# Kernel tuning notes

Measured on AMD Instinct MI355X. Metric: run time of the kernel, lower is better.

Reference implementation:

```python
import jax, jax.numpy as jnp
import numpy as np


def to_tb(r, size, base=4):
    # (B, size, size, size) -> (B, (size//base)^3, base, base, base)
    n = size // base
    r = r.reshape(-1, size, size, n, base)
    r = r.transpose(0, 1, 3, 2, 4)
    r = r.reshape(-1, size, n * n, base, base)
    r = r.transpose(0, 2, 1, 3, 4)
    return r.reshape(-1, n ** 3, base, base, base)


def from_tb(r, size, base=4):
    # inverse-ish of to_tb, ends with an extra (0,1,3,2) transpose as in source
    n = size // base
    r = r.reshape(-1, n * n, size, base, base)
    r = r.transpose(0, 2, 1, 3, 4)
    r = r.reshape(-1, size, size, n, base)
    r = r.transpose(0, 1, 3, 2, 4)
    r = r.reshape(-1, size, size, size)
    return r.transpose(0, 1, 3, 2)


def downscale(r, size):
    r = to_tb(r, size)  # base=4
    r = r.sum(axis=(2, 3, 4)) / 64.0
    r = r.reshape(-1, size // 4, size // 4, size // 4)
    return r.transpose(0, 3, 2, 1)


def setup_inputs() -> dict:
    key = jax.random.key(0)
    # (batch=2, level=4, 4, 4, 4^(3*4-2)) with 4*4*1048576 = 256^3 per slice
    x = jax.random.normal(key, (2, 4, 4, 4, 1048576), dtype=jnp.float32)
    return {"x": x}


def reference(x):
    level = x.shape[1]
    xt = jnp.transpose(x, (1, 0, 2, 3, 4))  # (level, batch, 4, 4, ...)
    batch = xt.shape[1]
    d2 = xt.shape[2]
    size_full = 4 ** level
    n3 = (4 ** (level - 1)) ** 3
    ret = []
    for i in range(level):
        r = xt[i]
        r = from_tb(r, size_full, 4 ** i)  # -> (batch, size, size, size)
        for k in range(i):
            r = downscale(r, 4 ** (level - k))
        for _ in range(i):
            r = jnp.tile(r, (1, 4, 4, 4))
        r = to_tb(r, size_full)  # (batch, n3, 4, 4, 4)
        ret.append(r.reshape(-1, n3, 64))
    out = jnp.stack(ret)  # (level, batch, n3, 64)
    out = out.transpose(1, 0, 2, 3).reshape(batch, -1, d2 ** 3)
    return out
```

## Files before the change

kernel.cpp:

```cpp
#include <hip/hip_runtime.h>


typedef float f4 __attribute__((ext_vector_type(4)));

__global__ __launch_bounds__(256) void k_reduce(const float* __restrict__ in,
                                                float* __restrict__ d1,
                                                float* __restrict__ p2,
                                                float* __restrict__ p3) {
    const int b = blockIdx.y;
    const int bx = blockIdx.x;
    const int tid = threadIdx.x;
    __shared__ float red[64];
    const f4* in4 = (const f4*)in;

    if (bx < 2048) {
        const int tlow = bx >> 1;
        const int kh = bx & 1;
        const long base4 = (long)b * 16777216 + 4194304;
        float acc[2] = {0.f, 0.f};
        for (int dz = 0; dz < 4; ++dz) {
            long rb = base4 + (long)(dz * 1024 + tlow) * 1024;
#pragma unroll
            for (int kk = 0; kk < 2; ++kk) {
                f4 v = __builtin_nontemporal_load(&in4[rb + (kh * 2 + kk) * 256 + tid]);
                acc[kk] += v.x + v.y + v.z + v.w;
            }
        }
#pragma unroll
        for (int kk = 0; kk < 2; ++kk) {
            acc[kk] += __shfl_xor(acc[kk], 4);
            acc[kk] += __shfl_xor(acc[kk], 8);
        }
        if ((tid & 12) == 0) {
            int yp = tlow >> 4;
            int zp = ((tlow & 15) << 2) + (tid & 3);
#pragma unroll
            for (int kk = 0; kk < 2; ++kk) {
                int xp = (kh * 2 + kk) * 16 + (tid >> 4);
                d1[b * 262144 + xp * 4096 + yp * 64 + zp] = acc[kk] * (1.0f / 64.0f);
            }
        }
    } else if (bx < 4096) {
        const int blk = bx - 2048;
        const int g = blk & 7, cell = blk >> 3;
        const int yp = cell >> 4, xp = cell & 15;
        const long base4 = (long)b * 16777216 + 2 * 4194304 + yp * 16384 + xp * 1024;
        float acc = 0.f;
        for (int dzi = 0; dzi < 2; ++dzi) {
            long rb = base4 + (long)(g * 2 + dzi) * 262144;
#pragma unroll
            for (int k = 0; k < 4; ++k) {
                f4 v = __builtin_nontemporal_load(&in4[rb + k * 256 + tid]);
                acc += v.x + v.y + v.z + v.w;
            }
        }
        acc += __shfl_xor(acc, 1);
        acc += __shfl_xor(acc, 2);
        if ((tid & 3) == 0) red[tid >> 2] = acc;
        __syncthreads();
        if (tid < 16) {
            float s = red[tid] + red[16 + tid] + red[32 + tid] + red[48 + tid];
            p2[(b * 8 + g) * 4096 + xp * 256 + yp * 16 + tid] = s;
        }
    } else {
        const int blk = bx - 4096;
        const int kc = blk & 7;
        const int orig = blk >> 3;
        const int xp = orig >> 6, hi = (orig >> 2) & 15, dxg = orig & 3;
        const long base4 = (long)b * 16777216 + 3 * 4194304 +
                           (long)hi * 262144 + xp * 65536 + dxg * 16384;
        float acc = 0.f;
        for (int kk = 0; kk < 8; ++kk) {
            f4 v = __builtin_nontemporal_load(&in4[base4 + (kc * 8 + kk) * 256 + tid]);
            acc += v.x + v.y + v.z + v.w;
        }
        acc += __shfl_xor(acc, 1);
        acc += __shfl_xor(acc, 2);
        acc += __shfl_xor(acc, 4);
        acc += __shfl_xor(acc, 8);
        if ((tid & 15) == 0) red[tid >> 4] = acc;
        __syncthreads();
        if (tid < 16) {
            int G = (hi * 4 + dxg) * 8 + kc;
            p3[((b * 4 + xp) * 512 + G) * 16 + tid] = red[tid];
        }
    }
}

__global__ __launch_bounds__(256) void k_combine(const float* __restrict__ p2,
                                                 const float* __restrict__ p3,
                                                 float* __restrict__ d2,
                                                 float* __restrict__ d3) {
    const int bid = blockIdx.x;
    const int tid = threadIdx.x;
    if (bid < 32) {
        int idx = bid * 256 + tid;
        int b = idx >> 12, r = idx & 4095;
        float s = 0.f;
#pragma unroll
        for (int g = 0; g < 8; ++g) s += p2[(b * 8 + g) * 4096 + r];
        d2[idx] = s * (1.0f / 4096.0f);
    } else {
        int v = bid - 32;
        int b = v >> 2, xp = v & 3;
        int c = tid & 15, gp = tid >> 4;
        const float* pb = p3 + (long)((b * 4 + xp) * 512) * 16 + c;
        float s = 0.f;
#pragma unroll
        for (int j = 0; j < 32; ++j) s += pb[(gp * 32 + j) * 16];
        __shared__ float red[256];
        red[gp * 16 + c] = s;
        __syncthreads();
        if (tid < 16) {
            float t = 0.f;
#pragma unroll
            for (int g = 0; g < 16; ++g) t += red[g * 16 + tid];
            d3[b * 64 + xp * 16 + tid] = t * (1.0f / 262144.0f);
        }
    }
}

__global__ __launch_bounds__(256) void k_perm(const float* __restrict__ in,
                                              float* __restrict__ out) {
    const int b = blockIdx.y;
    const int Y_hi = blockIdx.x >> 6, Z_hi = blockIdx.x & 63;
    const int tid = threadIdx.x;
    __shared__ float lds[16 * 260];
    const f4* in4 = (const f4*)in;
    f4* out4 = (f4*)out;
    const long in_b4 = (long)b * 16777216;
#pragma unroll
    for (int k = 0; k < 4; ++k) {
        int idx = k * 256 + tid;
        int r = idx >> 6;
        int col4 = idx & 63;
        int Y = Y_hi * 4 + (r >> 2), Z = Z_hi * 4 + (r & 3);
        f4 v = __builtin_nontemporal_load(&in4[in_b4 + (long)Y * 16384 + Z * 64 + col4]);
        *(f4*)&lds[r * 260 + col4 * 4] = v;
    }
    __syncthreads();
    const long out_b4 = (long)b * 16777216 + (long)Z_hi * 65536 + Y_hi * 1024;
#pragma unroll
    for (int k = 0; k < 4; ++k) {
        int idx = k * 256 + tid;
        int X = ((idx >> 4) << 2) + ((tid >> 2) & 3);
        int row0 = (tid & 3) * 4;
        f4 v;
        v.x = lds[(row0 + 0) * 260 + X];
        v.y = lds[(row0 + 1) * 260 + X];
        v.z = lds[(row0 + 2) * 260 + X];
        v.w = lds[(row0 + 3) * 260 + X];
        __builtin_nontemporal_store(v, &out4[out_b4 + idx]);
    }
}

__global__ __launch_bounds__(256) void k_bcast(const float* __restrict__ d1,
                                               const float* __restrict__ d2,
                                               const float* __restrict__ d3,
                                               float* __restrict__ out) {
    const int b = blockIdx.y;
    const int bx = blockIdx.x;
    const int tid = threadIdx.x;
    f4* out4 = (f4*)out;

    if (bx < 4096) {
        const f4* d14 = (const f4*)d1;
        const long ob = (long)b * 16777216 + 4194304;
        const int d1b = b * 65536;
#pragma unroll
        for (int k = 0; k < 4; ++k) {
            int o4 = bx * 1024 + k * 256 + tid;
            int u = o4 >> 4;
            int Xl = (o4 >> 2) & 3, Yl = o4 & 3;
            int Xh = u & 63, Yh = (u >> 6) & 63, Zh = u >> 12;
            int x = (Xh & 15) * 4 + Xl, y = (Yh & 15) * 4 + Yl;
            f4 v = d14[d1b + x * 1024 + y * 16 + (Zh & 15)];
            __builtin_nontemporal_store(v, &out4[ob + o4]);
        }
    } else if (bx < 8192) {
        const int blk = bx - 4096;
        const f4* d24 = (const f4*)d2;
        const long ob = (long)b * 16777216 + 2 * 4194304;
#pragma unroll
        for (int k = 0; k < 4; ++k) {
            int o4 = blk * 1024 + k * 256 + tid;
            int u = o4 >> 4;
            int Xl = (o4 >> 2) & 3, Yl = o4 & 3;
            int Xh = u & 63, Yh = (u >> 6) & 63, Zh = u >> 12;
            int x = (Xh & 3) * 4 + Xl, y = (Yh & 3) * 4 + Yl;
            f4 v = d24[b * 1024 + x * 64 + y * 4 + (Zh & 3)];
            __builtin_nontemporal_store(v, &out4[ob + o4]);
        }
    } else {
        const int blk = bx - 8192;
        const f4* d34 = (const f4*)d3;
        const f4 v = d34[b * 16 + (tid & 15)];
        const long ob = (long)b * 16777216 + 3 * 4194304;
#pragma unroll
        for (int k = 0; k < 4; ++k)
            __builtin_nontemporal_store(v, &out4[ob + blk * 1024 + k * 256 + tid]);
    }
}

extern "C" void kernel_launch(void* const* d_in, const int* in_sizes, int n_in,
                              void* d_out, int out_size, void* d_ws, size_t ws_size,
                              hipStream_t stream) {
    const float* in = (const float*)d_in[0];
    float* out = (float*)d_out;
    float* ws = (float*)d_ws;
    float* d1 = ws;
    float* p2 = ws + 524288;
    float* p3 = ws + 524288 + 65536;
    float* d2 = ws + 524288 + 65536 + 65536;
    float* d3 = ws + 524288 + 65536 + 65536 + 8192;
    k_reduce <<<dim3(6144, 2),  256, 0, stream>>>(in, d1, p2, p3);
    k_combine<<<40, 256, 0, stream>>>(p2, p3, d2, d3);
    k_perm   <<<dim3(4096, 2),  256, 0, stream>>>(in, out);
    k_bcast  <<<dim3(12288, 2), 256, 0, stream>>>(d1, d2, d3, out);
}
```

Measured before the change: 187.1 us.

## Fuse perm with combine and store downscaled data in broadcast-ready layout

Merges the small combine kernel into the permutation kernel as extra blocks, cutting one launch and letting the tiny reductions run alongside the large transpose. The d1 and d2 intermediates are now written in the layout the broadcast kernel consumes, so each broadcast block loads one contiguous f4 per thread and reuses it across its four stores, replacing per-element gathered index arithmetic. The d1 writes in the reduce kernel become more scattered in exchange.

```diff
diff --git a/kernel.cpp b/kernel.cpp
--- a/kernel.cpp
+++ b/kernel.cpp
@@ -37,7 +37,9 @@
 #pragma unroll
             for (int kk = 0; kk < 2; ++kk) {
                 int xp = (kh * 2 + kk) * 16 + (tid >> 4);
-                d1[b * 262144 + xp * 4096 + yp * 64 + zp] = acc[kk] * (1.0f / 64.0f);
+                int f4i = (zp >> 2) * 4096 + (yp >> 2) * 256 +
+                          (xp >> 2) * 16 + (xp & 3) * 4 + (yp & 3);
+                d1[b * 262144 + f4i * 4 + (zp & 3)] = acc[kk] * (1.0f / 64.0f);
             }
         }
     } else if (bx < 4096) {
@@ -87,28 +89,64 @@
     }
 }
 
-__global__ __launch_bounds__(256) void k_combine(const float* __restrict__ p2,
-                                                 const float* __restrict__ p3,
-                                                 float* __restrict__ d2,
-                                                 float* __restrict__ d3) {
-    const int bid = blockIdx.x;
+__global__ __launch_bounds__(256) void k_permcomb(const float* __restrict__ in,
+                                                  float* __restrict__ out,
+                                                  const float* __restrict__ p2,
+                                                  const float* __restrict__ p3,
+                                                  float* __restrict__ d2,
+                                                  float* __restrict__ d3) {
+    const int bx = blockIdx.x;
     const int tid = threadIdx.x;
-    if (bid < 32) {
-        int idx = bid * 256 + tid;
+    __shared__ float smem[16 * 260];
+
+    if (bx < 8192) {
+        const int b = bx >> 12;
+        const int rem = bx & 4095;
+        const int Y_hi = rem >> 6, Z_hi = rem & 63;
+        const f4* in4 = (const f4*)in;
+        f4* out4 = (f4*)out;
+        const long in_b4 = (long)b * 16777216;
+#pragma unroll
+        for (int k = 0; k < 4; ++k) {
+            int idx = k * 256 + tid;
+            int r = idx >> 6;
+            int col4 = idx & 63;
+            int Y = Y_hi * 4 + (r >> 2), Z = Z_hi * 4 + (r & 3);
+            f4 v = __builtin_nontemporal_load(&in4[in_b4 + (long)Y * 16384 + Z * 64 + col4]);
+            *(f4*)&smem[r * 260 + col4 * 4] = v;
+        }
+        __syncthreads();
+        const long out_b4 = (long)b * 16777216 + (long)Z_hi * 65536 + Y_hi * 1024;
+#pragma unroll
+        for (int k = 0; k < 4; ++k) {
+            int idx = k * 256 + tid;
+            int X = ((idx >> 4) << 2) + ((tid >> 2) & 3);
+            int row0 = (tid & 3) * 4;
+            f4 v;
+            v.x = smem[(row0 + 0) * 260 + X];
+            v.y = smem[(row0 + 1) * 260 + X];
+            v.z = smem[(row0 + 2) * 260 + X];
+            v.w = smem[(row0 + 3) * 260 + X];
+            __builtin_nontemporal_store(v, &out4[out_b4 + idx]);
+        }
+    } else if (bx < 8224) {
+        int idx = (bx - 8192) * 256 + tid;
         int b = idx >> 12, r = idx & 4095;
+        int xp = r >> 8, yp = (r >> 4) & 15, zp = r & 15;
         float s = 0.f;
 #pragma unroll
         for (int g = 0; g < 8; ++g) s += p2[(b * 8 + g) * 4096 + r];
-        d2[idx] = s * (1.0f / 4096.0f);
+        int f4i = (zp >> 2) * 256 + (yp >> 2) * 64 + (xp >> 2) * 16 + (xp & 3) * 4 + (yp & 3);
+        d2[b * 4096 + f4i * 4 + (zp & 3)] = s * (1.0f / 4096.0f);
     } else {
-        int v = bid - 32;
+        int v = bx - 8224;
         int b = v >> 2, xp = v & 3;
         int c = tid & 15, gp = tid >> 4;
         const float* pb = p3 + (long)((b * 4 + xp) * 512) * 16 + c;
         float s = 0.f;
 #pragma unroll
         for (int j = 0; j < 32; ++j) s += pb[(gp * 32 + j) * 16];
-        __shared__ float red[256];
+        float* red = smem;
         red[gp * 16 + c] = s;
         __syncthreads();
         if (tid < 16) {
@@ -117,40 +155,6 @@
             for (int g = 0; g < 16; ++g) t += red[g * 16 + tid];
             d3[b * 64 + xp * 16 + tid] = t * (1.0f / 262144.0f);
         }
-    }
-}
-
-__global__ __launch_bounds__(256) void k_perm(const float* __restrict__ in,
-                                              float* __restrict__ out) {
-    const int b = blockIdx.y;
-    const int Y_hi = blockIdx.x >> 6, Z_hi = blockIdx.x & 63;
-    const int tid = threadIdx.x;
-    __shared__ float lds[16 * 260];
-    const f4* in4 = (const f4*)in;
-    f4* out4 = (f4*)out;
-    const long in_b4 = (long)b * 16777216;
-#pragma unroll
-    for (int k = 0; k < 4; ++k) {
-        int idx = k * 256 + tid;
-        int r = idx >> 6;
-        int col4 = idx & 63;
-        int Y = Y_hi * 4 + (r >> 2), Z = Z_hi * 4 + (r & 3);
-        f4 v = __builtin_nontemporal_load(&in4[in_b4 + (long)Y * 16384 + Z * 64 + col4]);
-        *(f4*)&lds[r * 260 + col4 * 4] = v;
-    }
-    __syncthreads();
-    const long out_b4 = (long)b * 16777216 + (long)Z_hi * 65536 + Y_hi * 1024;
-#pragma unroll
-    for (int k = 0; k < 4; ++k) {
-        int idx = k * 256 + tid;
-        int X = ((idx >> 4) << 2) + ((tid >> 2) & 3);
-        int row0 = (tid & 3) * 4;
-        f4 v;
-        v.x = lds[(row0 + 0) * 260 + X];
-        v.y = lds[(row0 + 1) * 260 + X];
-        v.z = lds[(row0 + 2) * 260 + X];
-        v.w = lds[(row0 + 3) * 260 + X];
-        __builtin_nontemporal_store(v, &out4[out_b4 + idx]);
     }
 }
 
@@ -165,32 +169,19 @@
 
     if (bx < 4096) {
         const f4* d14 = (const f4*)d1;
+        const f4 v = d14[b * 65536 + ((bx >> 6) & 15) * 4096 + (bx & 15) * 256 + tid];
         const long ob = (long)b * 16777216 + 4194304;
-        const int d1b = b * 65536;
-#pragma unroll
-        for (int k = 0; k < 4; ++k) {
-            int o4 = bx * 1024 + k * 256 + tid;
-            int u = o4 >> 4;
-            int Xl = (o4 >> 2) & 3, Yl = o4 & 3;
-            int Xh = u & 63, Yh = (u >> 6) & 63, Zh = u >> 12;
-            int x = (Xh & 15) * 4 + Xl, y = (Yh & 15) * 4 + Yl;
-            f4 v = d14[d1b + x * 1024 + y * 16 + (Zh & 15)];
-            __builtin_nontemporal_store(v, &out4[ob + o4]);
-        }
+#pragma unroll
+        for (int k = 0; k < 4; ++k)
+            __builtin_nontemporal_store(v, &out4[ob + bx * 1024 + k * 256 + tid]);
     } else if (bx < 8192) {
         const int blk = bx - 4096;
         const f4* d24 = (const f4*)d2;
+        const f4 v = d24[b * 1024 + ((blk >> 6) & 3) * 256 + (blk & 3) * 64 + (tid & 63)];
         const long ob = (long)b * 16777216 + 2 * 4194304;
 #pragma unroll
-        for (int k = 0; k < 4; ++k) {
-            int o4 = blk * 1024 + k * 256 + tid;
-            int u = o4 >> 4;
-            int Xl = (o4 >> 2) & 3, Yl = o4 & 3;
-            int Xh = u & 63, Yh = (u >> 6) & 63, Zh = u >> 12;
-            int x = (Xh & 3) * 4 + Xl, y = (Yh & 3) * 4 + Yl;
-            f4 v = d24[b * 1024 + x * 64 + y * 4 + (Zh & 3)];
-            __builtin_nontemporal_store(v, &out4[ob + o4]);
-        }
+        for (int k = 0; k < 4; ++k)
+            __builtin_nontemporal_store(v, &out4[ob + blk * 1024 + k * 256 + tid]);
     } else {
         const int blk = bx - 8192;
         const f4* d34 = (const f4*)d3;
@@ -213,8 +204,7 @@
     float* p3 = ws + 524288 + 65536;
     float* d2 = ws + 524288 + 65536 + 65536;
     float* d3 = ws + 524288 + 65536 + 65536 + 8192;
-    k_reduce <<<dim3(6144, 2),  256, 0, stream>>>(in, d1, p2, p3);
-    k_combine<<<40, 256, 0, stream>>>(p2, p3, d2, d3);
-    k_perm   <<<dim3(4096, 2),  256, 0, stream>>>(in, out);
-    k_bcast  <<<dim3(12288, 2), 256, 0, stream>>>(d1, d2, d3, out);
-}
+    k_reduce  <<<dim3(6144, 2),  256, 0, stream>>>(in, d1, p2, p3);
+    k_permcomb<<<dim3(8232),     256, 0, stream>>>(in, out, p2, p3, d2, d3);
+    k_bcast   <<<dim3(12288, 2), 256, 0, stream>>>(d1, d2, d3, out);
+}
```

Result: faster. 182.5 us (-2.5%).
